# Kernel tuning notes

Hardware: AMD Instinct MI355X
Metric: run time of the kernel (lower is better)

Reference implementation:

```python
import jax, jax.numpy as jnp
import numpy as np

T_THR = 2.0   # temperature for threshold softmax over teachers
T_KD = 20.0   # KD temperature
ALPHA = 0.8   # KD mixing coefficient


def setup_inputs() -> dict:
    key = jax.random.key(0)
    ks = jax.random.split(key, 10)
    B, C = 4096, 1000
    d = {f"outputs{i+1}": jax.random.normal(ks[i], (B, C), dtype=jnp.float32) for i in range(8)}
    d["out_s"] = jax.random.normal(ks[8], (B, C), dtype=jnp.float32)
    d["targets"] = jax.random.randint(ks[9], (B,), 0, C, dtype=jnp.int64)
    return d


def reference(outputs1, outputs2, outputs3, outputs4, outputs5, outputs6, outputs7, outputs8, out_s, targets):
    outs = jnp.stack([outputs1, outputs2, outputs3, outputs4,
                      outputs5, outputs6, outputs7, outputs8])      # [8,B,C]
    mimic = outs.mean(axis=0)                                       # [B,C]
    all9 = jnp.concatenate([outs, mimic[None]], axis=0)             # [9,B,C]

    # per-(teacher,sample) top-2 margin, zero if target is not the argmax
    top2, _ = jax.lax.top_k(all9, 2)                                # [9,B,2]
    tgt_logit = jnp.take_along_axis(all9, targets[None, :, None], axis=2)[..., 0]  # [9,B]
    margin = jnp.where(tgt_logit == top2[..., 0], top2[..., 0] - top2[..., 1], 0.0)  # [9,B]
    thr = jax.nn.softmax(margin / T_THR, axis=0)                    # [9,B] softmax over 9 teachers

    max_preds = outs.max()                                          # scalar over the 8 teachers

    # cross-entropy of student (same for every teacher branch)
    logp_s = jax.nn.log_softmax(out_s, axis=-1)                     # [B,C]
    CE = -jnp.take_along_axis(logp_s, targets[:, None], axis=1)[:, 0]  # [B]

    # KD term per teacher
    logp_sT = jax.nn.log_softmax(out_s / T_KD, axis=-1)             # [B,C]
    p_tT = jax.nn.softmax(all9 / T_KD, axis=-1)                     # [9,B,C]
    KD = -jnp.sum(p_tT * logp_sT[None], axis=-1) * (T_KD * T_KD)    # [9,B]

    # dynamic per-sample weights
    w = tgt_logit / max_preds                                       # [9,B]
    loss = (1.0 - ALPHA * w) * CE[None] + ALPHA * w * KD            # [9,B]

    return jnp.sum(thr * loss, axis=0).mean()
```

## Files before the change

### kernel.cpp

```cpp
#include <hip/hip_runtime.h>

constexpr int   B        = 4096;
constexpr int   C        = 1000;
constexpr float ALPHA    = 0.8f;
constexpr float INV_TKD  = 0.05f;
constexpr float TKD2     = 400.0f;
constexpr float INV_TTHR = 0.5f;
constexpr float SENT     = -1e30f;

struct Part { float cand, mx, Z, Sd; };

__global__ __launch_bounds__(256, 4) void row_kernel(
    const float* __restrict__ T0, const float* __restrict__ T1,
    const float* __restrict__ T2, const float* __restrict__ T3,
    const float* __restrict__ T4, const float* __restrict__ T5,
    const float* __restrict__ T6, const float* __restrict__ T7,
    const float* __restrict__ S,  const int* __restrict__ TGT,
    float* __restrict__ ws_ce, float* __restrict__ ws_g, float* __restrict__ ws_m)
{
    const int lane = threadIdx.x & 63;
    const int wid  = threadIdx.x >> 6;
    const int b    = blockIdx.x * 4 + wid;
    const size_t base = (size_t)b * C;

    const int tgt   = TGT[b];
    const int uidx  = ((tgt >> 8) << 2) | (tgt & 3);
    const int slane = (tgt >> 2) & 63;

    auto load_row = [&](const float* __restrict__ p, float (&v)[16]) {
        const float4* p4 = (const float4*)(p + base);
#pragma unroll
        for (int k = 0; k < 4; ++k) {
            const int  idx = lane + 64 * k;
            const bool ok  = (k < 3) || (lane < 58);
            float4 f = p4[ok ? idx : 0];
            v[4*k+0] = ok ? f.x : SENT;
            v[4*k+1] = ok ? f.y : SENT;
            v[4*k+2] = ok ? f.z : SENT;
            v[4*k+3] = ok ? f.w : SENT;
        }
    };

    auto extract = [&](const float (&v)[16]) -> float {
        float cand = 0.0f;
#pragma unroll
        for (int i = 0; i < 16; ++i) cand = (i == uidx) ? v[i] : cand;
        return __shfl(cand, slane, 64);
    };

    float sv[16];
    load_row(S, sv);

    float buf[2][16];
    load_row(T0, buf[0]);

    float z1 = 0.0f, zT = 0.0f;
#pragma unroll
    for (int i = 0; i < 16; ++i) {
        z1 += __expf(sv[i]);
        zT += __expf(sv[i] * INV_TKD);
    }
#pragma unroll
    for (int m = 1; m < 64; m <<= 1) {
        z1 += __shfl_xor(z1, m, 64);
        zT += __shfl_xor(zT, m, 64);
    }
    const float logZ1 = __logf(z1);
    const float logZT = __logf(zT);
    const float s_tgt = extract(sv);
    const float ce    = logZ1 - s_tgt;

    float acc[16];
#pragma unroll
    for (int i = 0; i < 16; ++i) acc[i] = 0.0f;

    float rowmax8 = SENT;
    float s1 = 0.0f, s2 = 0.0f;

    auto partials = [&](const float (&v)[16]) -> Part {
        float cand = 0.0f, m_all = SENT, m_ex = SENT, Z = 0.0f, Sd = 0.0f;
#pragma unroll
        for (int i = 0; i < 16; ++i) {
            const float x = v[i];
            cand  = (i == uidx) ? x : cand;
            m_all = fmaxf(m_all, x);
            m_ex  = fmaxf(m_ex, (i == uidx) ? SENT : x);
            const float e = __expf(x * INV_TKD);
            Z += e;
            Sd = fmaf(e, sv[i], Sd);
        }
        Part p;
        p.cand = cand;
        p.mx   = (lane == slane) ? m_ex : m_all;
        p.Z    = Z;
        p.Sd   = Sd;
        return p;
    };

    auto finish = [&](Part p) -> float {
        float mx = p.mx, Z = p.Z, Sd = p.Sd;
#pragma unroll
        for (int m = 1; m < 64; m <<= 1) {
            mx  = fmaxf(mx, __shfl_xor(mx, m, 64));
            Z  += __shfl_xor(Z,  m, 64);
            Sd += __shfl_xor(Sd, m, 64);
        }
        const float tval   = __shfl(p.cand, slane, 64);
        const float margin = fmaxf(tval - mx, 0.0f);
        const float kd     = TKD2 * (logZT - INV_TKD * __fdividef(Sd, Z));
        const float u      = tval * (kd - ce);
        const float w8     = __expf(margin * INV_TTHR);
        s1 += w8;
        s2  = fmaf(w8, u, s2);
        return fmaxf(mx, tval);
    };

    const float* ptrs[8] = {T0, T1, T2, T3, T4, T5, T6, T7};
    Part P[2];

#pragma unroll
    for (int i = 0; i < 16; ++i) acc[i] += buf[0][i];
    P[0] = partials(buf[0]);
    load_row(T1, buf[1]);

#pragma unroll
    for (int t = 1; t < 8; ++t) {
        if (t + 1 < 8)
            load_row(ptrs[t + 1], buf[(t + 1) & 1]);
        rowmax8 = fmaxf(rowmax8, finish(P[(t - 1) & 1]));
        const float (&cv)[16] = buf[t & 1];
#pragma unroll
        for (int i = 0; i < 16; ++i) acc[i] += cv[i];
        P[t & 1] = partials(cv);
    }
    rowmax8 = fmaxf(rowmax8, finish(P[1]));

#pragma unroll
    for (int i = 0; i < 16; ++i) acc[i] *= 0.125f;
    finish(partials(acc));

    if (lane == 0) {
        ws_ce[b] = ce;
        ws_g[b]  = s2 / s1;
        ws_m[b]  = rowmax8;
    }
}

__global__ __launch_bounds__(256) void fin_kernel(
    const float* __restrict__ ce, const float* __restrict__ g,
    const float* __restrict__ m, float* __restrict__ out)
{
    __shared__ float  smax[4];
    __shared__ double ssum[4];
    const int tid  = threadIdx.x;
    const int lane = tid & 63;
    const int wid  = tid >> 6;

    float mx = SENT;
    for (int i = tid; i < B; i += 256) mx = fmaxf(mx, m[i]);
#pragma unroll
    for (int k = 1; k < 64; k <<= 1) mx = fmaxf(mx, __shfl_xor(mx, k, 64));
    if (lane == 0) smax[wid] = mx;
    __syncthreads();
    const float scale =
        ALPHA / fmaxf(fmaxf(smax[0], smax[1]), fmaxf(smax[2], smax[3]));

    double acc = 0.0;
    for (int i = tid; i < B; i += 256) acc += (double)(ce[i] + g[i] * scale);
#pragma unroll
    for (int k = 1; k < 64; k <<= 1) acc += __shfl_xor(acc, k, 64);
    if (lane == 0) ssum[wid] = acc;
    __syncthreads();
    if (tid == 0)
        out[0] = (float)((ssum[0] + ssum[1] + ssum[2] + ssum[3]) *
                         (1.0 / (double)B));
}

extern "C" void kernel_launch(void* const* d_in, const int* in_sizes, int n_in,
                              void* d_out, int out_size, void* d_ws, size_t ws_size,
                              hipStream_t stream)
{
    const float* T0 = (const float*)d_in[0];
    const float* T1 = (const float*)d_in[1];
    const float* T2 = (const float*)d_in[2];
    const float* T3 = (const float*)d_in[3];
    const float* T4 = (const float*)d_in[4];
    const float* T5 = (const float*)d_in[5];
    const float* T6 = (const float*)d_in[6];
    const float* T7 = (const float*)d_in[7];
    const float* S  = (const float*)d_in[8];
    const int*   TG = (const int*)d_in[9];

    float* ws = (float*)d_ws;
    float* ws_ce = ws;
    float* ws_g  = ws + B;
    float* ws_m  = ws + 2 * B;

    row_kernel<<<B / 4, 256, 0, stream>>>(T0, T1, T2, T3, T4, T5, T6, T7,
                                          S, TG, ws_ce, ws_g, ws_m);
    fin_kernel<<<1, 256, 0, stream>>>(ws_ce, ws_g, ws_m, (float*)d_out);
}
```

Before: 184.8 us.

## Split each row across two wavefronts and fuse final reduction via atomics

Each row is now handled by two wavefronts, each covering half the columns. Per-teacher partial reductions are exchanged through shared memory with a block barrier per teacher. The separate finalize kernel is replaced by double atomics, an ordered-key atomicMax, and a last-block-done counter, with a memset added to clear the accumulators. This halves per-thread register arrays so occupancy can rise (launch bounds raised to 6), at the cost of extra __syncthreads, global atomic contention and nondeterministic summation order.

```diff
diff --git a/kernel.cpp b/kernel.cpp
--- a/kernel.cpp
+++ b/kernel.cpp
@@ -8,31 +8,42 @@
 constexpr float INV_TTHR = 0.5f;
 constexpr float SENT     = -1e30f;
 
-struct Part { float cand, mx, Z, Sd; };
-
-__global__ __launch_bounds__(256, 4) void row_kernel(
+struct P4 { float mx, Z, Sd, tv; };
+
+__global__ __launch_bounds__(256, 6) void fused_kernel(
     const float* __restrict__ T0, const float* __restrict__ T1,
     const float* __restrict__ T2, const float* __restrict__ T3,
     const float* __restrict__ T4, const float* __restrict__ T5,
     const float* __restrict__ T6, const float* __restrict__ T7,
     const float* __restrict__ S,  const int* __restrict__ TGT,
-    float* __restrict__ ws_ce, float* __restrict__ ws_g, float* __restrict__ ws_m)
+    double* __restrict__ acc_ce, double* __restrict__ acc_g,
+    unsigned* __restrict__ max_key, unsigned* __restrict__ ctr,
+    float* __restrict__ out)
 {
-    const int lane = threadIdx.x & 63;
-    const int wid  = threadIdx.x >> 6;
-    const int b    = blockIdx.x * 4 + wid;
-    const size_t base = (size_t)b * C;
-
-    const int tgt   = TGT[b];
-    const int uidx  = ((tgt >> 8) << 2) | (tgt & 3);
-    const int slane = (tgt >> 2) & 63;
-
-    auto load_row = [&](const float* __restrict__ p, float (&v)[16]) {
+    __shared__ float4 xch[2][4];
+    __shared__ float4 xst[4];
+    __shared__ float4 xfin[2];
+
+    const int tid  = threadIdx.x;
+    const int lane = tid & 63;
+    const int wid  = tid >> 6;
+    const int rix  = wid >> 1;
+    const int h    = wid & 1;
+    const int row  = blockIdx.x * 2 + rix;
+    const size_t base = (size_t)row * C;
+
+    const int  tgt   = TGT[row];
+    const int  ftgt  = tgt >> 2;
+    const bool own   = (h == (ftgt >> 7));
+    const int  uidx  = (((ftgt >> 6) & 1) << 2) | (tgt & 3);
+    const int  slane = ftgt & 63;
+
+    auto load_half = [&](const float* __restrict__ p, float (&v)[8]) {
         const float4* p4 = (const float4*)(p + base);
 #pragma unroll
-        for (int k = 0; k < 4; ++k) {
-            const int  idx = lane + 64 * k;
-            const bool ok  = (k < 3) || (lane < 58);
+        for (int k = 0; k < 2; ++k) {
+            const int  idx = lane + 128 * h + 64 * k;
+            const bool ok  = (h == 0) || (k == 0) || (lane < 58);
             float4 f = p4[ok ? idx : 0];
             v[4*k+0] = ok ? f.x : SENT;
             v[4*k+1] = ok ? f.y : SENT;
@@ -41,46 +52,15 @@
         }
     };
 
-    auto extract = [&](const float (&v)[16]) -> float {
-        float cand = 0.0f;
-#pragma unroll
-        for (int i = 0; i < 16; ++i) cand = (i == uidx) ? v[i] : cand;
-        return __shfl(cand, slane, 64);
-    };
-
-    float sv[16];
-    load_row(S, sv);
-
-    float buf[2][16];
-    load_row(T0, buf[0]);
-
-    float z1 = 0.0f, zT = 0.0f;
-#pragma unroll
-    for (int i = 0; i < 16; ++i) {
-        z1 += __expf(sv[i]);
-        zT += __expf(sv[i] * INV_TKD);
-    }
-#pragma unroll
-    for (int m = 1; m < 64; m <<= 1) {
-        z1 += __shfl_xor(z1, m, 64);
-        zT += __shfl_xor(zT, m, 64);
-    }
-    const float logZ1 = __logf(z1);
-    const float logZT = __logf(zT);
-    const float s_tgt = extract(sv);
-    const float ce    = logZ1 - s_tgt;
-
-    float acc[16];
-#pragma unroll
-    for (int i = 0; i < 16; ++i) acc[i] = 0.0f;
-
-    float rowmax8 = SENT;
-    float s1 = 0.0f, s2 = 0.0f;
-
-    auto partials = [&](const float (&v)[16]) -> Part {
+    float sv[8];
+    load_half(S, sv);
+    float buf[2][8];
+    load_half(T0, buf[0]);
+
+    auto part_reduce = [&](const float (&v)[8]) -> P4 {
         float cand = 0.0f, m_all = SENT, m_ex = SENT, Z = 0.0f, Sd = 0.0f;
 #pragma unroll
-        for (int i = 0; i < 16; ++i) {
+        for (int i = 0; i < 8; ++i) {
             const float x = v[i];
             cand  = (i == uidx) ? x : cand;
             m_all = fmaxf(m_all, x);
@@ -89,91 +69,115 @@
             Z += e;
             Sd = fmaf(e, sv[i], Sd);
         }
-        Part p;
-        p.cand = cand;
-        p.mx   = (lane == slane) ? m_ex : m_all;
-        p.Z    = Z;
-        p.Sd   = Sd;
-        return p;
-    };
-
-    auto finish = [&](Part p) -> float {
-        float mx = p.mx, Z = p.Z, Sd = p.Sd;
+        float mx = (own && lane == slane) ? m_ex : m_all;
 #pragma unroll
         for (int m = 1; m < 64; m <<= 1) {
             mx  = fmaxf(mx, __shfl_xor(mx, m, 64));
             Z  += __shfl_xor(Z,  m, 64);
             Sd += __shfl_xor(Sd, m, 64);
         }
-        const float tval   = __shfl(p.cand, slane, 64);
-        const float margin = fmaxf(tval - mx, 0.0f);
-        const float kd     = TKD2 * (logZT - INV_TKD * __fdividef(Sd, Z));
-        const float u      = tval * (kd - ce);
-        const float w8     = __expf(margin * INV_TTHR);
+        float tv = __shfl(cand, slane, 64);
+        P4 p; p.mx = mx; p.Z = Z; p.Sd = Sd; p.tv = own ? tv : SENT;
+        return p;
+    };
+
+    float z1 = 0.0f, zT = 0.0f, scand = 0.0f;
+#pragma unroll
+    for (int i = 0; i < 8; ++i) {
+        z1 += __expf(sv[i]);
+        zT += __expf(sv[i] * INV_TKD);
+        scand = (i == uidx) ? sv[i] : scand;
+    }
+#pragma unroll
+    for (int m = 1; m < 64; m <<= 1) {
+        z1 += __shfl_xor(z1, m, 64);
+        zT += __shfl_xor(zT, m, 64);
+    }
+    float stv = __shfl(scand, slane, 64);
+    stv = own ? stv : SENT;
+    if (lane == 0) xst[wid] = make_float4(z1, zT, stv, 0.0f);
+
+    float acc[8];
+#pragma unroll
+    for (int i = 0; i < 8; ++i) acc[i] = buf[0][i];
+
+    P4 Preg[2];
+    Preg[0] = part_reduce(buf[0]);
+    if (lane == 0) xch[0][wid] = make_float4(Preg[0].mx, Preg[0].Z,
+                                             Preg[0].Sd, Preg[0].tv);
+    load_half(T1, buf[1]);
+    __syncthreads();
+
+    {
+        float4 o = xst[wid ^ 1];
+        z1 += o.x; zT += o.y; stv = fmaxf(stv, o.z);
+    }
+    const float logZT = __logf(zT);
+    const float ce    = __logf(z1) - stv;
+
+    float s1 = 0.0f, s2 = 0.0f, rowmax8 = SENT;
+    auto fin = [&](const P4& p, int par, bool upd) {
+        const float4 o = xch[par][wid ^ 1];
+        const float mx = fmaxf(p.mx, o.x);
+        const float Z  = p.Z + o.y;
+        const float Sd = p.Sd + o.z;
+        const float tv = fmaxf(p.tv, o.w);
+        const float margin = fmaxf(tv - mx, 0.0f);
+        const float kd = TKD2 * (logZT - INV_TKD * __fdividef(Sd, Z));
+        const float u  = tv * (kd - ce);
+        const float w8 = __expf(margin * INV_TTHR);
         s1 += w8;
         s2  = fmaf(w8, u, s2);
-        return fmaxf(mx, tval);
+        if (upd) rowmax8 = fmaxf(rowmax8, fmaxf(mx, tv));
     };
 
     const float* ptrs[8] = {T0, T1, T2, T3, T4, T5, T6, T7};
-    Part P[2];
-
-#pragma unroll
-    for (int i = 0; i < 16; ++i) acc[i] += buf[0][i];
-    P[0] = partials(buf[0]);
-    load_row(T1, buf[1]);
-
 #pragma unroll
     for (int t = 1; t < 8; ++t) {
         if (t + 1 < 8)
-            load_row(ptrs[t + 1], buf[(t + 1) & 1]);
-        rowmax8 = fmaxf(rowmax8, finish(P[(t - 1) & 1]));
-        const float (&cv)[16] = buf[t & 1];
-#pragma unroll
-        for (int i = 0; i < 16; ++i) acc[i] += cv[i];
-        P[t & 1] = partials(cv);
-    }
-    rowmax8 = fmaxf(rowmax8, finish(P[1]));
-
-#pragma unroll
-    for (int i = 0; i < 16; ++i) acc[i] *= 0.125f;
-    finish(partials(acc));
-
-    if (lane == 0) {
-        ws_ce[b] = ce;
-        ws_g[b]  = s2 / s1;
-        ws_m[b]  = rowmax8;
-    }
-}
-
-__global__ __launch_bounds__(256) void fin_kernel(
-    const float* __restrict__ ce, const float* __restrict__ g,
-    const float* __restrict__ m, float* __restrict__ out)
-{
-    __shared__ float  smax[4];
-    __shared__ double ssum[4];
-    const int tid  = threadIdx.x;
-    const int lane = tid & 63;
-    const int wid  = tid >> 6;
-
-    float mx = SENT;
-    for (int i = tid; i < B; i += 256) mx = fmaxf(mx, m[i]);
-#pragma unroll
-    for (int k = 1; k < 64; k <<= 1) mx = fmaxf(mx, __shfl_xor(mx, k, 64));
-    if (lane == 0) smax[wid] = mx;
+            load_half(ptrs[t + 1], buf[(t + 1) & 1]);
+        fin(Preg[(t - 1) & 1], (t - 1) & 1, true);
+        const float (&cv)[8] = buf[t & 1];
+#pragma unroll
+        for (int i = 0; i < 8; ++i) acc[i] += cv[i];
+        Preg[t & 1] = part_reduce(cv);
+        if (lane == 0) xch[t & 1][wid] = make_float4(Preg[t & 1].mx, Preg[t & 1].Z,
+                                                     Preg[t & 1].Sd, Preg[t & 1].tv);
+        __syncthreads();
+    }
+    fin(Preg[1], 1, true);
+
+#pragma unroll
+    for (int i = 0; i < 8; ++i) acc[i] *= 0.125f;
+    Preg[0] = part_reduce(acc);
+    if (lane == 0) xch[0][wid] = make_float4(Preg[0].mx, Preg[0].Z,
+                                             Preg[0].Sd, Preg[0].tv);
     __syncthreads();
-    const float scale =
-        ALPHA / fmaxf(fmaxf(smax[0], smax[1]), fmaxf(smax[2], smax[3]));
-
-    double acc = 0.0;
-    for (int i = tid; i < B; i += 256) acc += (double)(ce[i] + g[i] * scale);
-#pragma unroll
-    for (int k = 1; k < 64; k <<= 1) acc += __shfl_xor(acc, k, 64);
-    if (lane == 0) ssum[wid] = acc;
+    fin(Preg[0], 0, false);
+
+    const float g = s2 / s1;
+    if (h == 0 && lane == 0) xfin[rix] = make_float4(ce, g, rowmax8, 0.0f);
     __syncthreads();
-    if (tid == 0)
-        out[0] = (float)((ssum[0] + ssum[1] + ssum[2] + ssum[3]) *
-                         (1.0 / (double)B));
+    if (tid == 0) {
+        const float4 a = xfin[0], b4 = xfin[1];
+        atomicAdd(acc_ce, (double)a.x + (double)b4.x);
+        atomicAdd(acc_g,  (double)a.y + (double)b4.y);
+        const float    mrow = fmaxf(a.z, b4.z);
+        const unsigned u    = __float_as_uint(mrow);
+        const unsigned key  = (u & 0x80000000u) ? ~u : (u | 0x80000000u);
+        atomicMax(max_key, key);
+        __threadfence();
+        const unsigned old = atomicAdd(ctr, 1u);
+        if (old == gridDim.x - 1) {
+            const double   ces = atomicAdd(acc_ce, 0.0);
+            const double   gs  = atomicAdd(acc_g,  0.0);
+            const unsigned mk  = atomicOr(max_key, 0u);
+            const unsigned mu  = (mk & 0x80000000u) ? (mk ^ 0x80000000u) : ~mk;
+            const float maxp  = __uint_as_float(mu);
+            const float scale = ALPHA / maxp;
+            out[0] = (float)((ces + (double)scale * gs) * (1.0 / (double)B));
+        }
+    }
 }
 
 extern "C" void kernel_launch(void* const* d_in, const int* in_sizes, int n_in,
@@ -191,12 +195,13 @@
     const float* S  = (const float*)d_in[8];
     const int*   TG = (const int*)d_in[9];
 
-    float* ws = (float*)d_ws;
-    float* ws_ce = ws;
-    float* ws_g  = ws + B;
-    float* ws_m  = ws + 2 * B;
-
-    row_kernel<<<B / 4, 256, 0, stream>>>(T0, T1, T2, T3, T4, T5, T6, T7,
-                                          S, TG, ws_ce, ws_g, ws_m);
-    fin_kernel<<<1, 256, 0, stream>>>(ws_ce, ws_g, ws_m, (float*)d_out);
+    double*   acc_ce  = (double*)d_ws;
+    double*   acc_g   = acc_ce + 1;
+    unsigned* max_key = (unsigned*)(acc_g + 1);
+    unsigned* ctr     = max_key + 1;
+
+    hipMemsetAsync(d_ws, 0, 32, stream);
+    fused_kernel<<<B / 2, 256, 0, stream>>>(T0, T1, T2, T3, T4, T5, T6, T7,
+                                            S, TG, acc_ce, acc_g, max_key, ctr,
+                                            (float*)d_out);
 }
```

After: 329.1 us. +78.1%, slower.
